# Optimization experiments

Measured on AMD Instinct MI355X. Metric: run time of the kernel, lower is better.

## Reference

```python
import jax, jax.numpy as jnp
import numpy as np

N_ATOM, N_QUERY, KNN = 100000, 20000, 32
E = N_QUERY * KNN
HID, EDGE_F, HEADS = 128, 16, 8
D_HEAD = HID // HEADS
LN_EPS = 1e-5


def setup_inputs() -> dict:
    key = jax.random.key(0)
    ks = jax.random.split(key, 16)
    s = 1.0 / np.sqrt(HID)
    src = jax.random.randint(ks[0], (E,), 0, N_ATOM)
    dst = jnp.repeat(jnp.arange(N_QUERY), KNN)  # each query has KNN incoming edges
    return {
        "h_atom": jax.random.normal(ks[1], (N_ATOM, HID), jnp.float32),
        "h_query": jax.random.normal(ks[2], (N_QUERY, HID), jnp.float32),
        "edge_attr": jax.random.uniform(ks[3], (E, EDGE_F), jnp.float32),
        "W_q": jax.random.normal(ks[4], (HID, HID), jnp.float32) * s,
        "W_k": jax.random.normal(ks[5], (HID, HID), jnp.float32) * s,
        "W_v": jax.random.normal(ks[6], (HID, HID), jnp.float32) * s,
        "W_rbf": jax.random.normal(ks[7], (HEADS, EDGE_F), jnp.float32) * (1.0 / np.sqrt(EDGE_F)),
        "W1": jax.random.normal(ks[8], (HID, 2 * HID), jnp.float32) * (1.0 / np.sqrt(2 * HID)),
        "b1": jnp.zeros((HID,), jnp.float32),
        "W2": jax.random.normal(ks[9], (HID, HID), jnp.float32) * s,
        "b2": jnp.zeros((HID,), jnp.float32),
        "ln_gamma": jnp.ones((HID,), jnp.float32),
        "ln_beta": jnp.zeros((HID,), jnp.float32),
        "edge_index": jnp.stack([src, dst]),
        "n_query": N_QUERY,
    }


def reference(h_atom, h_query, edge_attr, W_q, W_k, W_v, W_rbf, W1, b1, W2, b2,
              ln_gamma, ln_beta, edge_index, n_query):
    src, dst = edge_index[0], edge_index[1]
    En = src.shape[0]
    # gather + project, per-edge multi-head Q/K/V  [E, H, d]
    Q = (h_query[dst] @ W_q.T).reshape(En, HEADS, D_HEAD)
    K = (h_atom[src] @ W_k.T).reshape(En, HEADS, D_HEAD)
    V = (h_atom[src] @ W_v.T).reshape(En, HEADS, D_HEAD)
    scores = jnp.einsum("ehd,ehd->eh", Q, K) / np.sqrt(D_HEAD) + edge_attr @ W_rbf.T  # [E,H]
    # segment softmax over edges sharing the same dst query, per head
    seg_max = jax.lax.stop_gradient(jax.ops.segment_max(scores, dst, num_segments=n_query))
    ex = jnp.exp(scores - seg_max[dst])
    denom = jax.ops.segment_sum(ex, dst, num_segments=n_query)
    alpha = ex / (denom[dst] + 1e-16)  # [E,H]
    # weighted scatter-add aggregation
    msgs = (alpha[:, :, None] * V).reshape(En, HID)
    agg = jax.ops.segment_sum(msgs, dst, num_segments=n_query)  # [Nq, HID]
    # update MLP + residual + LayerNorm
    z = jnp.concatenate([h_query, agg], axis=-1)
    delta = jax.nn.relu(z @ W1.T + b1) @ W2.T + b2
    y = h_query + delta
    mu = y.mean(-1, keepdims=True)
    var = y.var(-1, keepdims=True)
    return (y - mu) / jnp.sqrt(var + LN_EPS) * ln_gamma + ln_beta
```

## Files before the change

kernel.cpp:

```cpp
#include <hip/hip_runtime.h>
#include <hip/hip_bf16.h>
#include <math.h>

#define N_ATOM   100000
#define N_QUERY  20000
#define KNN      32

typedef __attribute__((ext_vector_type(8))) short  short8;
typedef __attribute__((ext_vector_type(4))) float  floatx4;
typedef __attribute__((ext_vector_type(2))) float  fx2;

static __device__ __forceinline__ unsigned short f2bf_bits(float f) {
  union { __hip_bfloat16 h; unsigned short u; } cv;
  cv.h = __float2bfloat16(f);
  return cv.u;
}
static __device__ __forceinline__ float bflo(unsigned int u) { return __uint_as_float(u << 16); }
static __device__ __forceinline__ float bfhi(unsigned int u) { return __uint_as_float(u & 0xffff0000u); }

__global__ void pack_all_kernel(const float* __restrict__ Wq, const float* __restrict__ Wk,
                                const float* __restrict__ Wv, const float* __restrict__ W1,
                                const float* __restrict__ W2,
                                unsigned short* __restrict__ WKVp, unsigned short* __restrict__ WQp,
                                unsigned short* __restrict__ W1p,  unsigned short* __restrict__ W2p) {
  int tid = blockIdx.x * blockDim.x + threadIdx.x;
  if (tid >= 98304) return;
  const float *Wa, *Wb; int nsplit, Kd, Nd; unsigned short* dst; float scale = 1.0f;
  int t = tid;
  if (t < 32768)      { Wa = Wk; Wb = Wv; nsplit = 128; Kd = 128; Nd = 256; dst = WKVp; }
  else if (t < 49152) { t -= 32768; Wa = Wq; Wb = Wq; nsplit = 128; Kd = 128; Nd = 128; dst = WQp; scale = 0.25f; }
  else if (t < 81920) { t -= 49152; Wa = W1; Wb = W1; nsplit = 128; Kd = 256; Nd = 128; dst = W1p; }
  else                { t -= 81920; Wa = W2; Wb = W2; nsplit = 128; Kd = 128; Nd = 128; dst = W2p; }
  int j    = t & 7;
  int lane = (t >> 3) & 63;
  int t2   = t >> 9;
  int NT   = Nd >> 4;
  int ntile = t2 % NT;
  int ktile = t2 / NT;
  int k = ktile * 32 + (lane >> 4) * 8 + j;
  int n = ntile * 16 + (lane & 15);
  float v = (n < nsplit) ? Wa[(size_t)n * Kd + k] : Wb[(size_t)(n - nsplit) * Kd + k];
  dst[t] = f2bf_bits(v * scale);
}

template<int KD, int NT, int EPI>
__global__ __launch_bounds__(256) void gemm_k(
    const float* __restrict__ A, const unsigned short* __restrict__ Bp, int M,
    unsigned short* __restrict__ outb, unsigned char* __restrict__ outp8) {
  constexpr int ND = NT * 16;
  constexpr int LDSB = (EPI == 3) ? 24576 : 16;
  __shared__ char lds[LDSB];
  const int l    = threadIdx.x & 63;
  const int w    = threadIdx.x >> 6;
  const int quad = l >> 4;
  const int col0 = l & 15;
  const int row0 = blockIdx.x * 64 + w * 16;
  int arow = row0 + col0;
  if (arow >= M) arow = M - 1;

  floatx4 acc[NT];
#pragma unroll
  for (int i = 0; i < NT; i++) acc[i] = (floatx4){0.f, 0.f, 0.f, 0.f};

  const float* aptr = A + (size_t)arow * KD + quad * 8;
#pragma unroll
  for (int k0 = 0; k0 < KD; k0 += 32) {
    floatx4 a0 = *(const floatx4*)(aptr + k0);
    floatx4 a1 = *(const floatx4*)(aptr + k0 + 4);
    short8 af;
    af[0] = (short)f2bf_bits(a0[0]); af[1] = (short)f2bf_bits(a0[1]);
    af[2] = (short)f2bf_bits(a0[2]); af[3] = (short)f2bf_bits(a0[3]);
    af[4] = (short)f2bf_bits(a1[0]); af[5] = (short)f2bf_bits(a1[1]);
    af[6] = (short)f2bf_bits(a1[2]); af[7] = (short)f2bf_bits(a1[3]);
    const unsigned short* bbase = Bp + (size_t)(k0 >> 5) * NT * 512 + l * 8;
#pragma unroll
    for (int nt = 0; nt < NT; nt++) {
      short8 bf = *(const short8*)(bbase + nt * 512);
      acc[nt] = __builtin_amdgcn_mfma_f32_16x16x32_bf16(af, bf, acc[nt], 0, 0, 0);
    }
  }

  if (EPI == 0) {
#pragma unroll
    for (int nt = 0; nt < NT; nt++) {
#pragma unroll
      for (int r = 0; r < 4; r++) {
        int row = row0 + quad * 4 + r;
        if (row < M) outb[(size_t)row * ND + nt * 16 + col0] = f2bf_bits(acc[nt][r]);
      }
    }
  } else {
#pragma unroll
    for (int nt = 0; nt < NT; nt++) {
#pragma unroll
      for (int r = 0; r < 4; r++) {
        int rl = w * 16 + quad * 4 + r;
        int c  = nt * 16 + col0;
        if (c < 128) {
          int pk = __builtin_amdgcn_cvt_pk_fp8_f32(acc[nt][r], acc[nt][r], 0, false);
          lds[rl * 128 + c] = (char)(pk & 0xff);
        } else {
          *(unsigned short*)&lds[8192 + rl * 256 + (c - 128) * 2] = f2bf_bits(acc[nt][r]);
        }
      }
    }
    __syncthreads();
    const int row0g = blockIdx.x * 64;
#pragma unroll
    for (int it = 0; it < 2; it++) {
      int off = threadIdx.x * 16 + it * 4096;
      if (row0g + (off >> 7) < M)
        *(float4*)(outp8 + (size_t)row0g * 128 + off) = *(const float4*)&lds[off];
    }
#pragma unroll
    for (int it = 0; it < 4; it++) {
      int off = threadIdx.x * 16 + it * 4096;
      if (row0g + (off >> 8) < M)
        *(float4*)((char*)outb + (size_t)row0g * 256 + off) = *(const float4*)&lds[8192 + off];
    }
  }
}

__global__ __launch_bounds__(256) void attn_kernel(
    const unsigned short* __restrict__ Qb,
    const unsigned char* __restrict__ Kp8,
    const unsigned short* __restrict__ Vb,
    const float* __restrict__ edge_attr,
    const float* __restrict__ Wrbf,
    const int* __restrict__ src,
    float* __restrict__ Agg) {
  const int l = threadIdx.x & 63;
  const int w = threadIdx.x >> 6;
  const int q = blockIdx.x * 4 + w;
  const int j = l >> 3;
  const int h = l & 7;

  const int e0 = q * KNN;
  int srcj = (l < KNN) ? src[e0 + l] : 0;

  float qd[16];
  {
    const unsigned int* qp = (const unsigned int*)(Qb + (size_t)q * 128 + h * 16);
#pragma unroll
    for (int i = 0; i < 8; i++) {
      unsigned int u = qp[i];
      qd[2 * i] = bflo(u); qd[2 * i + 1] = bfhi(u);
    }
  }
  float wr[16];
  {
    const float* wp = Wrbf + h * 16;
#pragma unroll
    for (int i = 0; i < 16; i++) wr[i] = wp[i];
  }

  float acc[16];
#pragma unroll
  for (int i = 0; i < 16; i++) acc[i] = 0.f;
  float lsum = 0.f;

#pragma unroll
  for (int p = 0; p < 4; p++) {
    const int e = p * 8 + j;
    int s = __shfl(srcj, e, 64);
    uint4 kq = *(const uint4*)(Kp8 + (size_t)s * 128 + h * 16);
    const uint4* vp = (const uint4*)(Vb + ((size_t)s * 128 + h * 16));
    uint4 v0 = vp[0], v1 = vp[1];
    const float4* ep = (const float4*)(edge_attr + (size_t)(e0 + e) * 16);
    float4 ea0 = ep[0], ea1 = ep[1], ea2 = ep[2], ea3 = ep[3];

    float kd = 0.f;
    {
      fx2 f0, f1;
      f0 = __builtin_amdgcn_cvt_pk_f32_fp8((int)kq.x, false);
      f1 = __builtin_amdgcn_cvt_pk_f32_fp8((int)kq.x, true);
      kd += qd[0] * f0[0] + qd[1] * f0[1] + qd[2] * f1[0] + qd[3] * f1[1];
      f0 = __builtin_amdgcn_cvt_pk_f32_fp8((int)kq.y, false);
      f1 = __builtin_amdgcn_cvt_pk_f32_fp8((int)kq.y, true);
      kd += qd[4] * f0[0] + qd[5] * f0[1] + qd[6] * f1[0] + qd[7] * f1[1];
      f0 = __builtin_amdgcn_cvt_pk_f32_fp8((int)kq.z, false);
      f1 = __builtin_amdgcn_cvt_pk_f32_fp8((int)kq.z, true);
      kd += qd[8] * f0[0] + qd[9] * f0[1] + qd[10] * f1[0] + qd[11] * f1[1];
      f0 = __builtin_amdgcn_cvt_pk_f32_fp8((int)kq.w, false);
      f1 = __builtin_amdgcn_cvt_pk_f32_fp8((int)kq.w, true);
      kd += qd[12] * f0[0] + qd[13] * f0[1] + qd[14] * f1[0] + qd[15] * f1[1];
    }
    float ed = wr[0]*ea0.x + wr[1]*ea0.y + wr[2]*ea0.z + wr[3]*ea0.w
             + wr[4]*ea1.x + wr[5]*ea1.y + wr[6]*ea1.z + wr[7]*ea1.w
             + wr[8]*ea2.x + wr[9]*ea2.y + wr[10]*ea2.z + wr[11]*ea2.w
             + wr[12]*ea3.x + wr[13]*ea3.y + wr[14]*ea3.z + wr[15]*ea3.w;

    float pe = __expf(kd + ed);
    lsum += pe;
    acc[0]  += pe * bflo(v0.x); acc[1]  += pe * bfhi(v0.x);
    acc[2]  += pe * bflo(v0.y); acc[3]  += pe * bfhi(v0.y);
    acc[4]  += pe * bflo(v0.z); acc[5]  += pe * bfhi(v0.z);
    acc[6]  += pe * bflo(v0.w); acc[7]  += pe * bfhi(v0.w);
    acc[8]  += pe * bflo(v1.x); acc[9]  += pe * bfhi(v1.x);
    acc[10] += pe * bflo(v1.y); acc[11] += pe * bfhi(v1.y);
    acc[12] += pe * bflo(v1.z); acc[13] += pe * bfhi(v1.z);
    acc[14] += pe * bflo(v1.w); acc[15] += pe * bfhi(v1.w);
  }

#pragma unroll
  for (int mask = 8; mask <= 32; mask <<= 1) {
    lsum += __shfl_xor(lsum, mask, 64);
#pragma unroll
    for (int i = 0; i < 16; i++) acc[i] += __shfl_xor(acc[i], mask, 64);
  }
  float inv = 1.f / (lsum + 1e-16f);
  float* dst = Agg + (size_t)q * 128 + h * 16;
  if (j == 0) {
    float4 o0 = {acc[0] * inv, acc[1] * inv, acc[2] * inv, acc[3] * inv};
    float4 o1 = {acc[4] * inv, acc[5] * inv, acc[6] * inv, acc[7] * inv};
    *(float4*)(dst)     = o0;
    *(float4*)(dst + 4) = o1;
  } else if (j == 1) {
    float4 o2 = {acc[8] * inv, acc[9] * inv, acc[10] * inv, acc[11] * inv};
    float4 o3 = {acc[12] * inv, acc[13] * inv, acc[14] * inv, acc[15] * inv};
    *(float4*)(dst + 8)  = o2;
    *(float4*)(dst + 12) = o3;
  }
}

__global__ __launch_bounds__(256) void mlp_kernel(
    const float* __restrict__ h_query, const float* __restrict__ Agg,
    const unsigned short* __restrict__ W1p, const unsigned short* __restrict__ W2p,
    const float* __restrict__ b1, const float* __restrict__ b2,
    const float* __restrict__ gamma, const float* __restrict__ beta,
    float* __restrict__ out) {
  constexpr int M = N_QUERY;
  constexpr int STRIDE = 136;
  __shared__ unsigned short hid[64 * STRIDE];

  const int l    = threadIdx.x & 63;
  const int w    = threadIdx.x >> 6;
  const int quad = l >> 4;
  const int col0 = l & 15;
  const int row0 = blockIdx.x * 64 + w * 16;
  int arow = row0 + col0;
  if (arow >= M) arow = M - 1;

  floatx4 acc[8];
#pragma unroll
  for (int i = 0; i < 8; i++) acc[i] = (floatx4){0.f, 0.f, 0.f, 0.f};
#pragma unroll
  for (int k0 = 0; k0 < 256; k0 += 32) {
    const float* sp = (k0 < 128) ? (h_query + (size_t)arow * 128 + k0)
                                 : (Agg + (size_t)arow * 128 + (k0 - 128));
    floatx4 a0 = *(const floatx4*)(sp + quad * 8);
    floatx4 a1 = *(const floatx4*)(sp + quad * 8 + 4);
    short8 af;
    af[0] = (short)f2bf_bits(a0[0]); af[1] = (short)f2bf_bits(a0[1]);
    af[2] = (short)f2bf_bits(a0[2]); af[3] = (short)f2bf_bits(a0[3]);
    af[4] = (short)f2bf_bits(a1[0]); af[5] = (short)f2bf_bits(a1[1]);
    af[6] = (short)f2bf_bits(a1[2]); af[7] = (short)f2bf_bits(a1[3]);
    const unsigned short* bbase = W1p + (size_t)(k0 >> 5) * 8 * 512 + l * 8;
#pragma unroll
    for (int nt = 0; nt < 8; nt++) {
      short8 bf = *(const short8*)(bbase + nt * 512);
      acc[nt] = __builtin_amdgcn_mfma_f32_16x16x32_bf16(af, bf, acc[nt], 0, 0, 0);
    }
  }
#pragma unroll
  for (int nt = 0; nt < 8; nt++) {
#pragma unroll
    for (int r = 0; r < 4; r++) {
      int rl = w * 16 + quad * 4 + r;
      float v = acc[nt][r] + b1[nt * 16 + col0];
      hid[rl * STRIDE + nt * 16 + col0] = f2bf_bits(fmaxf(v, 0.f));
    }
  }
  __syncthreads();

  floatx4 acc2[8];
#pragma unroll
  for (int i = 0; i < 8; i++) acc2[i] = (floatx4){0.f, 0.f, 0.f, 0.f};
  const int rloc = w * 16 + col0;
#pragma unroll
  for (int k0 = 0; k0 < 128; k0 += 32) {
    short8 af = *(const short8*)(hid + rloc * STRIDE + k0 + quad * 8);
    const unsigned short* bbase = W2p + (size_t)(k0 >> 5) * 8 * 512 + l * 8;
#pragma unroll
    for (int nt = 0; nt < 8; nt++) {
      short8 bf = *(const short8*)(bbase + nt * 512);
      acc2[nt] = __builtin_amdgcn_mfma_f32_16x16x32_bf16(af, bf, acc2[nt], 0, 0, 0);
    }
  }

#pragma unroll
  for (int r = 0; r < 4; r++) {
    int row = row0 + quad * 4 + r;
    int rr  = row < M ? row : M - 1;
    float v[8];
    float s1 = 0.f, s2 = 0.f;
#pragma unroll
    for (int nt = 0; nt < 8; nt++) {
      int c = nt * 16 + col0;
      v[nt] = acc2[nt][r] + b2[c] + h_query[(size_t)rr * 128 + c];
      s1 += v[nt];
    }
    s1 += __shfl_xor(s1, 1, 64); s1 += __shfl_xor(s1, 2, 64);
    s1 += __shfl_xor(s1, 4, 64); s1 += __shfl_xor(s1, 8, 64);
#pragma unroll
    for (int nt = 0; nt < 8; nt++) s2 += v[nt] * v[nt];
    s2 += __shfl_xor(s2, 1, 64); s2 += __shfl_xor(s2, 2, 64);
    s2 += __shfl_xor(s2, 4, 64); s2 += __shfl_xor(s2, 8, 64);
    float mean = s1 * (1.0f / 128.0f);
    float var  = s2 * (1.0f / 128.0f) - mean * mean;
    float rstd = rsqrtf(var + 1e-5f);
    if (row < M) {
#pragma unroll
      for (int nt = 0; nt < 8; nt++) {
        int c = nt * 16 + col0;
        out[(size_t)row * 128 + c] = (v[nt] - mean) * rstd * gamma[c] + beta[c];
      }
    }
  }
}

extern "C" void kernel_launch(void* const* d_in, const int* in_sizes, int n_in,
                              void* d_out, int out_size, void* d_ws, size_t ws_size,
                              hipStream_t stream) {
  const float* h_atom    = (const float*)d_in[0];
  const float* h_query   = (const float*)d_in[1];
  const float* edge_attr = (const float*)d_in[2];
  const float* W_q  = (const float*)d_in[3];
  const float* W_k  = (const float*)d_in[4];
  const float* W_v  = (const float*)d_in[5];
  const float* Wrbf = (const float*)d_in[6];
  const float* W1   = (const float*)d_in[7];
  const float* b1   = (const float*)d_in[8];
  const float* W2   = (const float*)d_in[9];
  const float* b2   = (const float*)d_in[10];
  const float* ln_g = (const float*)d_in[11];
  const float* ln_b = (const float*)d_in[12];
  const int* edge_index = (const int*)d_in[13];
  float* out = (float*)d_out;

  char* ws = (char*)d_ws;
  unsigned char*  Kp8 = (unsigned char*)(ws);
  unsigned short* Vb  = (unsigned short*)(ws + 12800000);
  unsigned short* Qb  = (unsigned short*)(ws + 38400000);
  float* Agg          = (float*)(ws + 43520000);
  unsigned short* WKVp = (unsigned short*)(ws + 53760000);
  unsigned short* WQp  = WKVp + 32768;
  unsigned short* W1p  = WQp  + 16384;
  unsigned short* W2p  = W1p  + 32768;

  pack_all_kernel<<<(98304 + 255) / 256, 256, 0, stream>>>(
      W_q, W_k, W_v, W1, W2, WKVp, WQp, W1p, W2p);

  gemm_k<128, 16, 3><<<(N_ATOM + 63) / 64, 256, 0, stream>>>(
      h_atom, WKVp, N_ATOM, Vb, Kp8);
  gemm_k<128, 8, 0><<<(N_QUERY + 63) / 64, 256, 0, stream>>>(
      h_query, WQp, N_QUERY, Qb, nullptr);
  attn_kernel<<<N_QUERY / 4, 256, 0, stream>>>(Qb, Kp8, Vb, edge_attr, Wrbf, edge_index, Agg);
  mlp_kernel<<<(N_QUERY + 63) / 64, 256, 0, stream>>>(
      h_query, Agg, W1p, W2p, b1, b2, ln_g, ln_b, out);
}
```

Baseline: 238.0 us.

## Store V projections in fp8 and merge KV and Q GEMMs into one launch

V is now quantized to fp8 like K, which halves V's storage and its gather traffic in the attention kernel. The V loads drop from two 16-byte reads to one, at the cost of fp8 unpack conversions. The separate K/V and Q projection GEMMs are fused into a single launch that branches on block index, removing one kernel launch and letting the two run concurrently. The trade-off is lower V precision, which raises accuracy risk.

```diff
diff --git a/kernel.cpp b/kernel.cpp
--- a/kernel.cpp
+++ b/kernel.cpp
@@ -43,65 +43,51 @@
   dst[t] = f2bf_bits(v * scale);
 }
 
-template<int KD, int NT, int EPI>
-__global__ __launch_bounds__(256) void gemm_k(
-    const float* __restrict__ A, const unsigned short* __restrict__ Bp, int M,
-    unsigned short* __restrict__ outb, unsigned char* __restrict__ outp8) {
-  constexpr int ND = NT * 16;
-  constexpr int LDSB = (EPI == 3) ? 24576 : 16;
-  __shared__ char lds[LDSB];
+__global__ __launch_bounds__(256) void gemm_kvq(
+    const float* __restrict__ h_atom, const float* __restrict__ h_query,
+    const unsigned short* __restrict__ WKVp, const unsigned short* __restrict__ WQp,
+    unsigned char* __restrict__ Kp8, unsigned char* __restrict__ Vp8,
+    unsigned short* __restrict__ Qb) {
+  constexpr int KB = (N_ATOM + 63) / 64;
+  __shared__ char lds[16384];
   const int l    = threadIdx.x & 63;
   const int w    = threadIdx.x >> 6;
   const int quad = l >> 4;
   const int col0 = l & 15;
-  const int row0 = blockIdx.x * 64 + w * 16;
-  int arow = row0 + col0;
-  if (arow >= M) arow = M - 1;
-
-  floatx4 acc[NT];
-#pragma unroll
-  for (int i = 0; i < NT; i++) acc[i] = (floatx4){0.f, 0.f, 0.f, 0.f};
-
-  const float* aptr = A + (size_t)arow * KD + quad * 8;
-#pragma unroll
-  for (int k0 = 0; k0 < KD; k0 += 32) {
-    floatx4 a0 = *(const floatx4*)(aptr + k0);
-    floatx4 a1 = *(const floatx4*)(aptr + k0 + 4);
-    short8 af;
-    af[0] = (short)f2bf_bits(a0[0]); af[1] = (short)f2bf_bits(a0[1]);
-    af[2] = (short)f2bf_bits(a0[2]); af[3] = (short)f2bf_bits(a0[3]);
-    af[4] = (short)f2bf_bits(a1[0]); af[5] = (short)f2bf_bits(a1[1]);
-    af[6] = (short)f2bf_bits(a1[2]); af[7] = (short)f2bf_bits(a1[3]);
-    const unsigned short* bbase = Bp + (size_t)(k0 >> 5) * NT * 512 + l * 8;
-#pragma unroll
-    for (int nt = 0; nt < NT; nt++) {
-      short8 bf = *(const short8*)(bbase + nt * 512);
-      acc[nt] = __builtin_amdgcn_mfma_f32_16x16x32_bf16(af, bf, acc[nt], 0, 0, 0);
-    }
-  }
-
-  if (EPI == 0) {
-#pragma unroll
-    for (int nt = 0; nt < NT; nt++) {
-#pragma unroll
-      for (int r = 0; r < 4; r++) {
-        int row = row0 + quad * 4 + r;
-        if (row < M) outb[(size_t)row * ND + nt * 16 + col0] = f2bf_bits(acc[nt][r]);
-      }
-    }
-  } else {
-#pragma unroll
-    for (int nt = 0; nt < NT; nt++) {
+
+  if ((int)blockIdx.x < KB) {
+    const int row0 = blockIdx.x * 64 + w * 16;
+    int arow = row0 + col0;
+    if (arow >= N_ATOM) arow = N_ATOM - 1;
+    floatx4 acc[16];
+#pragma unroll
+    for (int i = 0; i < 16; i++) acc[i] = (floatx4){0.f, 0.f, 0.f, 0.f};
+    const float* aptr = h_atom + (size_t)arow * 128 + quad * 8;
+#pragma unroll
+    for (int k0 = 0; k0 < 128; k0 += 32) {
+      floatx4 a0 = *(const floatx4*)(aptr + k0);
+      floatx4 a1 = *(const floatx4*)(aptr + k0 + 4);
+      short8 af;
+      af[0] = (short)f2bf_bits(a0[0]); af[1] = (short)f2bf_bits(a0[1]);
+      af[2] = (short)f2bf_bits(a0[2]); af[3] = (short)f2bf_bits(a0[3]);
+      af[4] = (short)f2bf_bits(a1[0]); af[5] = (short)f2bf_bits(a1[1]);
+      af[6] = (short)f2bf_bits(a1[2]); af[7] = (short)f2bf_bits(a1[3]);
+      const unsigned short* bbase = WKVp + (size_t)(k0 >> 5) * 16 * 512 + l * 8;
+#pragma unroll
+      for (int nt = 0; nt < 16; nt++) {
+        short8 bf = *(const short8*)(bbase + nt * 512);
+        acc[nt] = __builtin_amdgcn_mfma_f32_16x16x32_bf16(af, bf, acc[nt], 0, 0, 0);
+      }
+    }
+#pragma unroll
+    for (int nt = 0; nt < 16; nt++) {
 #pragma unroll
       for (int r = 0; r < 4; r++) {
         int rl = w * 16 + quad * 4 + r;
         int c  = nt * 16 + col0;
-        if (c < 128) {
-          int pk = __builtin_amdgcn_cvt_pk_fp8_f32(acc[nt][r], acc[nt][r], 0, false);
-          lds[rl * 128 + c] = (char)(pk & 0xff);
-        } else {
-          *(unsigned short*)&lds[8192 + rl * 256 + (c - 128) * 2] = f2bf_bits(acc[nt][r]);
-        }
+        int pk = __builtin_amdgcn_cvt_pk_fp8_f32(acc[nt][r], acc[nt][r], 0, false);
+        if (c < 128) lds[rl * 128 + c] = (char)(pk & 0xff);
+        else         lds[8192 + rl * 128 + (c - 128)] = (char)(pk & 0xff);
       }
     }
     __syncthreads();
@@ -109,14 +95,46 @@
 #pragma unroll
     for (int it = 0; it < 2; it++) {
       int off = threadIdx.x * 16 + it * 4096;
-      if (row0g + (off >> 7) < M)
-        *(float4*)(outp8 + (size_t)row0g * 128 + off) = *(const float4*)&lds[off];
-    }
-#pragma unroll
-    for (int it = 0; it < 4; it++) {
+      if (row0g + (off >> 7) < N_ATOM)
+        *(float4*)(Kp8 + (size_t)row0g * 128 + off) = *(const float4*)&lds[off];
+    }
+#pragma unroll
+    for (int it = 0; it < 2; it++) {
       int off = threadIdx.x * 16 + it * 4096;
-      if (row0g + (off >> 8) < M)
-        *(float4*)((char*)outb + (size_t)row0g * 256 + off) = *(const float4*)&lds[8192 + off];
+      if (row0g + (off >> 7) < N_ATOM)
+        *(float4*)(Vp8 + (size_t)row0g * 128 + off) = *(const float4*)&lds[8192 + off];
+    }
+  } else {
+    const int row0 = ((int)blockIdx.x - KB) * 64 + w * 16;
+    int arow = row0 + col0;
+    if (arow >= N_QUERY) arow = N_QUERY - 1;
+    floatx4 acc[8];
+#pragma unroll
+    for (int i = 0; i < 8; i++) acc[i] = (floatx4){0.f, 0.f, 0.f, 0.f};
+    const float* aptr = h_query + (size_t)arow * 128 + quad * 8;
+#pragma unroll
+    for (int k0 = 0; k0 < 128; k0 += 32) {
+      floatx4 a0 = *(const floatx4*)(aptr + k0);
+      floatx4 a1 = *(const floatx4*)(aptr + k0 + 4);
+      short8 af;
+      af[0] = (short)f2bf_bits(a0[0]); af[1] = (short)f2bf_bits(a0[1]);
+      af[2] = (short)f2bf_bits(a0[2]); af[3] = (short)f2bf_bits(a0[3]);
+      af[4] = (short)f2bf_bits(a1[0]); af[5] = (short)f2bf_bits(a1[1]);
+      af[6] = (short)f2bf_bits(a1[2]); af[7] = (short)f2bf_bits(a1[3]);
+      const unsigned short* bbase = WQp + (size_t)(k0 >> 5) * 8 * 512 + l * 8;
+#pragma unroll
+      for (int nt = 0; nt < 8; nt++) {
+        short8 bf = *(const short8*)(bbase + nt * 512);
+        acc[nt] = __builtin_amdgcn_mfma_f32_16x16x32_bf16(af, bf, acc[nt], 0, 0, 0);
+      }
+    }
+#pragma unroll
+    for (int nt = 0; nt < 8; nt++) {
+#pragma unroll
+      for (int r = 0; r < 4; r++) {
+        int row = row0 + quad * 4 + r;
+        if (row < N_QUERY) Qb[(size_t)row * 128 + nt * 16 + col0] = f2bf_bits(acc[nt][r]);
+      }
     }
   }
 }
@@ -124,7 +142,7 @@
 __global__ __launch_bounds__(256) void attn_kernel(
     const unsigned short* __restrict__ Qb,
     const unsigned char* __restrict__ Kp8,
-    const unsigned short* __restrict__ Vb,
+    const unsigned char* __restrict__ Vp8,
     const float* __restrict__ edge_attr,
     const float* __restrict__ Wrbf,
     const int* __restrict__ src,
@@ -164,8 +182,7 @@
     const int e = p * 8 + j;
     int s = __shfl(srcj, e, 64);
     uint4 kq = *(const uint4*)(Kp8 + (size_t)s * 128 + h * 16);
-    const uint4* vp = (const uint4*)(Vb + ((size_t)s * 128 + h * 16));
-    uint4 v0 = vp[0], v1 = vp[1];
+    uint4 vq = *(const uint4*)(Vp8 + (size_t)s * 128 + h * 16);
     const float4* ep = (const float4*)(edge_attr + (size_t)(e0 + e) * 16);
     float4 ea0 = ep[0], ea1 = ep[1], ea2 = ep[2], ea3 = ep[3];
 
@@ -192,14 +209,21 @@
 
     float pe = __expf(kd + ed);
     lsum += pe;
-    acc[0]  += pe * bflo(v0.x); acc[1]  += pe * bfhi(v0.x);
-    acc[2]  += pe * bflo(v0.y); acc[3]  += pe * bfhi(v0.y);
-    acc[4]  += pe * bflo(v0.z); acc[5]  += pe * bfhi(v0.z);
-    acc[6]  += pe * bflo(v0.w); acc[7]  += pe * bfhi(v0.w);
-    acc[8]  += pe * bflo(v1.x); acc[9]  += pe * bfhi(v1.x);
-    acc[10] += pe * bflo(v1.y); acc[11] += pe * bfhi(v1.y);
-    acc[12] += pe * bflo(v1.z); acc[13] += pe * bfhi(v1.z);
-    acc[14] += pe * bflo(v1.w); acc[15] += pe * bfhi(v1.w);
+    {
+      fx2 g0, g1;
+      g0 = __builtin_amdgcn_cvt_pk_f32_fp8((int)vq.x, false);
+      g1 = __builtin_amdgcn_cvt_pk_f32_fp8((int)vq.x, true);
+      acc[0] += pe * g0[0]; acc[1] += pe * g0[1]; acc[2] += pe * g1[0]; acc[3] += pe * g1[1];
+      g0 = __builtin_amdgcn_cvt_pk_f32_fp8((int)vq.y, false);
+      g1 = __builtin_amdgcn_cvt_pk_f32_fp8((int)vq.y, true);
+      acc[4] += pe * g0[0]; acc[5] += pe * g0[1]; acc[6] += pe * g1[0]; acc[7] += pe * g1[1];
+      g0 = __builtin_amdgcn_cvt_pk_f32_fp8((int)vq.z, false);
+      g1 = __builtin_amdgcn_cvt_pk_f32_fp8((int)vq.z, true);
+      acc[8] += pe * g0[0]; acc[9] += pe * g0[1]; acc[10] += pe * g1[0]; acc[11] += pe * g1[1];
+      g0 = __builtin_amdgcn_cvt_pk_f32_fp8((int)vq.w, false);
+      g1 = __builtin_amdgcn_cvt_pk_f32_fp8((int)vq.w, true);
+      acc[12] += pe * g0[0]; acc[13] += pe * g0[1]; acc[14] += pe * g1[0]; acc[15] += pe * g1[1];
+    }
   }
 
 #pragma unroll
@@ -340,10 +364,10 @@
 
   char* ws = (char*)d_ws;
   unsigned char*  Kp8 = (unsigned char*)(ws);
-  unsigned short* Vb  = (unsigned short*)(ws + 12800000);
-  unsigned short* Qb  = (unsigned short*)(ws + 38400000);
-  float* Agg          = (float*)(ws + 43520000);
-  unsigned short* WKVp = (unsigned short*)(ws + 53760000);
+  unsigned char*  Vp8 = (unsigned char*)(ws + 12800000);
+  unsigned short* Qb  = (unsigned short*)(ws + 25600000);
+  float* Agg          = (float*)(ws + 30720000);
+  unsigned short* WKVp = (unsigned short*)(ws + 40960000);
   unsigned short* WQp  = WKVp + 32768;
   unsigned short* W1p  = WQp  + 16384;
   unsigned short* W2p  = W1p  + 32768;
@@ -351,11 +375,12 @@
   pack_all_kernel<<<(98304 + 255) / 256, 256, 0, stream>>>(
       W_q, W_k, W_v, W1, W2, WKVp, WQp, W1p, W2p);
 
-  gemm_k<128, 16, 3><<<(N_ATOM + 63) / 64, 256, 0, stream>>>(
-      h_atom, WKVp, N_ATOM, Vb, Kp8);
-  gemm_k<128, 8, 0><<<(N_QUERY + 63) / 64, 256, 0, stream>>>(
-      h_query, WQp, N_QUERY, Qb, nullptr);
-  attn_kernel<<<N_QUERY / 4, 256, 0, stream>>>(Qb, Kp8, Vb, edge_attr, Wrbf, edge_index, Agg);
+  constexpr int KB = (N_ATOM + 63) / 64;
+  constexpr int QB = (N_QUERY + 63) / 64;
+  gemm_kvq<<<KB + QB, 256, 0, stream>>>(h_atom, h_query, WKVp, WQp, Kp8, Vp8, Qb);
+
+  attn_kernel<<<N_QUERY / 4, 256, 0, stream>>>(Qb, Kp8, Vp8, edge_attr, Wrbf, edge_index, Agg);
+
   mlp_kernel<<<(N_QUERY + 63) / 64, 256, 0, stream>>>(
       h_query, Agg, W1p, W2p, b1, b2, ln_g, ln_b, out);
 }
```

New measurement: 218.1 us. -8.3%, faster.
